# Kernel optimization log

Hardware: AMD Instinct MI355X
Metric: run time of the kernel (lower is better)

## Reference

```python
import jax, jax.numpy as jnp
import numpy as np

B, LV, LT, D, H = 32, 196, 40, 512, 8
DH = D // H


def setup_inputs() -> dict:
    key = jax.random.key(0)
    ks = jax.random.split(key, 10)
    s = 0.02
    return {
        "bef_feat": jax.random.normal(ks[0], (B, LV, D), jnp.float32),
        "sent_feat": jax.random.normal(ks[1], (B, LT, D), jnp.float32),
        "aft_feat": jax.random.normal(ks[2], (B, LV, D), jnp.float32),
        "masks": jnp.ones((B, LT), jnp.float32),
        "conv1_w": jax.random.normal(ks[3], (D, 2 * D), jnp.float32) * s,  # 1x1 conv: (out,in)
        "conv1_b": jnp.zeros((D,), jnp.float32),
        "in_proj_w": jax.random.normal(ks[4], (3 * D, D), jnp.float32) * s,
        "out_proj_w": jax.random.normal(ks[5], (D, D), jnp.float32) * s,
        "conv2_w": jax.random.normal(ks[6], (D, D), jnp.float32) * s,
        "conv2_b": jnp.zeros((D,), jnp.float32),
        "q_w": jax.random.normal(ks[7], (D, D), jnp.float32) * s,
        "q_b": jnp.zeros((D,), jnp.float32),
        "k_w": jax.random.normal(ks[8], (D, D), jnp.float32) * s,
        "k_b": jnp.zeros((D,), jnp.float32),
        "logit_scale": jnp.ones((), jnp.float32),
    }


def _forward(bef_feat, sent_feat, aft_feat, masks,
             conv1_w, conv1_b, in_proj_w, out_proj_w, conv2_w, conv2_b,
             q_w, q_b, k_w, k_b, logit_scale):
    batch, Lv, d = bef_feat.shape
    # masked text mean (plain mean over full length, as in original)
    sent = sent_feat * masks[:, :, None]
    sent_mean = jnp.mean(sent, axis=1)  # (B, D)
    # concat image grid feat with broadcast text feat -> 1x1 conv (conv1)
    img = jnp.transpose(bef_feat, (0, 2, 1))                       # (B, D, 196)
    txt = jnp.broadcast_to(sent_mean[:, :, None], (batch, d, Lv))  # (B, D, 196)
    v1 = jnp.concatenate([img, txt], axis=1)                       # (B, 2D, 196)
    v1 = jnp.einsum('bcl,oc->blo', v1, conv1_w) + conv1_b          # (B, 196, D)
    # multi-head self-attention over the 196 positions (no biases)
    qkv = jnp.einsum('bld,ed->ble', v1, in_proj_w)                 # (B, 196, 3D)
    q, k, v = jnp.split(qkv, 3, axis=-1)
    to_heads = lambda t: t.reshape(batch, Lv, H, DH).transpose(0, 2, 1, 3)
    q, k, v = to_heads(q), to_heads(k), to_heads(v)
    scores = jnp.einsum('bhld,bhmd->bhlm', q, k) / jnp.sqrt(jnp.float32(DH))
    attn = jax.nn.softmax(scores, axis=-1)
    o = jnp.einsum('bhlm,bhmd->bhld', attn, v)
    o = o.transpose(0, 2, 1, 3).reshape(batch, Lv, d)
    o = o @ out_proj_w.T
    # 1x1 conv (conv2)
    mod_img1 = jnp.einsum('bld,od->blo', o, conv2_w) + conv2_b     # (B, 196, D)
    # ContraAttention: cross-batch retrieval logits
    ql = (mod_img1 @ q_w.T + q_b).reshape(batch, Lv, H, DH).transpose(0, 2, 1, 3)  # (B,H,196,DH)
    kl = (aft_feat @ k_w.T + k_b).reshape(batch, Lv, H, DH).transpose(0, 2, 1, 3)  # (B,H,196,DH)
    logits = jnp.einsum('ahld,bhmd->ablm', ql, kl)                 # (B, B, 196, 196), sums over h,d
    # vid_mask and com_mask (attention_mask) are all-ones -> sums are Lv
    t2v = jnp.sum(jnp.max(logits, axis=-1), axis=2) / jnp.float32(Lv)  # (B, B)
    v2t = jnp.sum(jnp.max(logits, axis=-2), axis=2) / jnp.float32(Lv)  # (B, B)
    S = 0.5 * (t2v + v2t) * jnp.exp(logit_scale)
    cross_en = lambda m: -jnp.mean(jnp.diag(jax.nn.log_softmax(m, axis=-1)))
    return 0.5 * (cross_en(S) + cross_en(S.T))


def reference(bef_feat, sent_feat, aft_feat, masks,
              conv1_w, conv1_b, in_proj_w, out_proj_w, conv2_w, conv2_b,
              q_w, q_b, k_w, k_b, logit_scale):
    return _forward(bef_feat, sent_feat, aft_feat, masks,
                    conv1_w, conv1_b, in_proj_w, out_proj_w, conv2_w, conv2_b,
                    q_w, q_b, k_w, k_b, logit_scale)
```

## Files before the change

kernel.cpp:

```cpp
#include <hip/hip_runtime.h>


typedef unsigned int u32;
typedef unsigned short u16;
typedef __attribute__((ext_vector_type(8))) short bf16x8;
typedef __attribute__((ext_vector_type(4))) float f32x4;

#define DEV __device__ __forceinline__

DEV u16 f2bf(float f) {
  u32 u = __builtin_bit_cast(u32, f);
  u = (u + 0x7FFFu + ((u >> 16) & 1u)) >> 16;
  return (u16)u;
}
DEV float bf2f(u16 h) { u32 u = ((u32)h) << 16; return __builtin_bit_cast(float, u); }
DEV u32 encf(float f) { u32 u = __builtin_bit_cast(u32, f); return (u & 0x80000000u) ? ~u : (u | 0x80000000u); }
DEV float decf(u32 e) { u32 u = (e & 0x80000000u) ? (e & 0x7FFFFFFFu) : ~e; return __builtin_bit_cast(float, u); }

DEV void gll16(const u16* g, u16* l) {
  __builtin_amdgcn_global_load_lds(
      (const __attribute__((address_space(1))) void*)g,
      (__attribute__((address_space(3))) void*)l, 16, 0, 0);
}

#define VMCNT0 asm volatile("s_waitcnt vmcnt(0)" ::: "memory")
#define SBAR __builtin_amdgcn_s_barrier()

DEV void cast8(const float* __restrict__ in, u16* __restrict__ out, int i) {
  const float4* p = (const float4*)in + (size_t)i * 2;
  float4 a = p[0], b = p[1];
  u16 t[8] = {f2bf(a.x), f2bf(a.y), f2bf(a.z), f2bf(a.w),
              f2bf(b.x), f2bf(b.y), f2bf(b.z), f2bf(b.w)};
  *(uint4*)(out + (size_t)i * 8) = *(uint4*)t;
}

DEV void tcast(const float* __restrict__ in, u16* __restrict__ out, int t, int tid, float* sm) {
  int bx = t & 15, by = t >> 4;
  int tx = tid & 31, ty = tid >> 5;
  float (*tt)[33] = (float(*)[33])sm;
  for (int i = ty; i < 32; i += 8) tt[i][tx] = in[(size_t)(by * 32 + i) * 512 + bx * 32 + tx];
  __syncthreads();
  for (int i = ty; i < 32; i += 8) out[(size_t)(bx * 32 + i) * 512 + by * 32 + tx] = f2bf(tt[tx][i]);
}

__global__ __launch_bounds__(256) void k_prep(
    const float* __restrict__ bef, const float* __restrict__ aft,
    const float* __restrict__ sent, const float* __restrict__ masks,
    const float* __restrict__ conv1_w, const float* __restrict__ conv1_b,
    const float* __restrict__ in_proj_w, const float* __restrict__ out_proj_w,
    const float* __restrict__ conv2_w, const float* __restrict__ conv2_b,
    const float* __restrict__ q_w, const float* __restrict__ q_b,
    const float* __restrict__ k_w,
    u16* __restrict__ bef16, u16* __restrict__ aft16,
    u16* __restrict__ inproj16, u16* __restrict__ kw16, u16* __restrict__ qw16,
    u16* __restrict__ w1a16, u16* __restrict__ wcT16, u16* __restrict__ woT16,
    float* __restrict__ biasb, float* __restrict__ biasq,
    uint4* __restrict__ maxbuf) {
  __shared__ float smemf[1056];
  const int blk = blockIdx.x, tid = threadIdx.x;
  if (blk < 32) {
    int b = blk;
    float* sm = smemf;
    for (int d = tid; d < 512; d += 256) {
      float s = 0.f;
#pragma unroll 8
      for (int t = 0; t < 40; ++t) s += sent[(size_t)b * 40 * 512 + (size_t)t * 512 + d] * masks[b * 40 + t];
      sm[d] = s * (1.0f / 40.0f);
    }
    __syncthreads();
    for (int o = tid; o < 512; o += 256) {
      const float* wr = conv1_w + (size_t)o * 1024 + 512;
      float acc = conv1_b[o];
#pragma unroll 8
      for (int c = 0; c < 512; ++c) acc += sm[c] * wr[c];
      biasb[b * 512 + o] = acc;
    }
  } else if (blk < 424) {
    maxbuf[(size_t)(blk - 32) * 256 + tid] = (uint4){0u, 0u, 0u, 0u};
  } else if (blk < 426) {
    int j = (blk - 424) * 256 + tid;
    if (j < 512) {
      const float* wr = q_w + (size_t)j * 512;
      float acc = q_b[j];
#pragma unroll 8
      for (int d = 0; d < 512; ++d) acc += wr[d] * conv2_b[d];
      biasq[j] = acc;
    }
  } else if (blk < 1994) {
    cast8(bef, bef16, (blk - 426) * 256 + tid);
  } else if (blk < 3562) {
    cast8(aft, aft16, (blk - 1994) * 256 + tid);
  } else if (blk < 3946) {
    cast8(in_proj_w, inproj16, (blk - 3562) * 256 + tid);
  } else if (blk < 4074) {
    cast8(k_w, kw16, (blk - 3946) * 256 + tid);
  } else if (blk < 4202) {
    cast8(q_w, qw16, (blk - 4074) * 256 + tid);
  } else if (blk < 4330) {
    int i = (blk - 4202) * 256 + tid;
    int o = i >> 6, c0 = (i & 63) * 8;
    const float* p = conv1_w + (size_t)o * 1024 + c0;
    u16 t[8];
#pragma unroll
    for (int j = 0; j < 8; ++j) t[j] = f2bf(p[j]);
    *(uint4*)(w1a16 + (size_t)o * 512 + c0) = *(uint4*)t;
  } else if (blk < 4586) {
    tcast(conv2_w, wcT16, blk - 4330, tid, smemf);
  } else {
    tcast(out_proj_w, woT16, blk - 4586, tid, smemf);
  }
}

DEV void stage_gm(const u16* __restrict__ xb, const u16* __restrict__ wb,
                  u16* Xb, u16* Wb, int wave, int lane, int koff, int scol) {
  int r8 = lane >> 3;
#pragma unroll
  for (int i = 0; i < 6; ++i) {
    int s = wave + i * 4;
    if (s < 16) gll16(xb + (size_t)(s * 8 + r8) * 512 + koff + scol, Xb + s * 512);
    else        gll16(wb + (size_t)((s - 16) * 8 + r8) * 512 + koff + scol, Wb + (s - 16) * 512);
  }
}

DEV void comp_gm(const u16* Xb, const u16* Wb, int wave, int quad, int l15, int rsw,
                 f32x4 (&acc)[2][4]) {
#pragma unroll
  for (int kk = 0; kk < 64; kk += 32) {
    int co = (kk | (quad << 3)) ^ rsw;
    bf16x8 a0 = *(const bf16x8*)&Xb[(wave * 32 + l15) * 64 + co];
    bf16x8 a1 = *(const bf16x8*)&Xb[(wave * 32 + 16 + l15) * 64 + co];
#pragma unroll
    for (int nt = 0; nt < 4; ++nt) {
      bf16x8 b = *(const bf16x8*)&Wb[(nt * 16 + l15) * 64 + co];
      acc[0][nt] = __builtin_amdgcn_mfma_f32_16x16x32_bf16(a0, b, acc[0][nt], 0, 0, 0);
      acc[1][nt] = __builtin_amdgcn_mfma_f32_16x16x32_bf16(a1, b, acc[1][nt], 0, 0, 0);
    }
  }
}

__global__ __launch_bounds__(256) void k_gemm2(
    const u16* __restrict__ X1, const u16* __restrict__ W1, u16* __restrict__ o1,
    const float* __restrict__ b1, int nbx1, int N1, int m1, int nblk1,
    const u16* __restrict__ X2, const u16* __restrict__ W2, u16* __restrict__ o2,
    const float* __restrict__ b2, int nbx2, int N2, int m2) {
  __shared__ u16 Xl0[128 * 64], Xl1[128 * 64];
  __shared__ u16 Wl0[64 * 64],  Wl1[64 * 64];
  int g = blockIdx.x;
  const u16 *X, *W; u16* out; const float* bias; int N, biasMode, bx, by;
  if (g < nblk1) {
    X = X1; W = W1; out = o1; bias = b1; N = N1; biasMode = m1;
    bx = g % nbx1; by = g / nbx1;
  } else {
    g -= nblk1;
    X = X2; W = W2; out = o2; bias = b2; N = N2; biasMode = m2;
    bx = g % nbx2; by = g / nbx2;
  }
  int tid = threadIdx.x;
  int tileM = bx * 128, tileN = by * 64;
  int wave = tid >> 6, lane = tid & 63, quad = lane >> 4, l15 = lane & 15;
  const int rsw = (l15 & 7) << 3;
  const int scol = (((lane & 7) ^ ((lane >> 3) & 7)) << 3);
  f32x4 z = {0.f, 0.f, 0.f, 0.f};
  f32x4 acc[2][4] = {{z, z, z, z}, {z, z, z, z}};
  const u16* xb = X + (size_t)tileM * 512;
  const u16* wb = W + (size_t)tileN * 512;

  stage_gm(xb, wb, Xl0, Wl0, wave, lane, 0, scol);
  VMCNT0; SBAR;
#pragma unroll
  for (int kc = 0; kc < 8; kc += 2) {
    stage_gm(xb, wb, Xl1, Wl1, wave, lane, (kc + 1) * 64, scol);
    comp_gm(Xl0, Wl0, wave, quad, l15, rsw, acc);
    VMCNT0; SBAR;
    if (kc + 2 < 8)
      stage_gm(xb, wb, Xl0, Wl0, wave, lane, (kc + 2) * 64, scol);
    comp_gm(Xl1, Wl1, wave, quad, l15, rsw, acc);
    VMCNT0; SBAR;
  }
#pragma unroll
  for (int s = 0; s < 2; ++s) {
    int row0 = tileM + wave * 32 + s * 16 + quad * 4;
#pragma unroll
    for (int nt = 0; nt < 4; ++nt) {
      int col = tileN + nt * 16 + l15;
      float bv = (biasMode == 1) ? bias[col] : 0.0f;
#pragma unroll
      for (int r = 0; r < 4; ++r) {
        int row = row0 + r;
        float v = acc[s][nt][r] + bv;
        if (biasMode == 2) v += bias[(row / 196) * 512 + col];
        out[(size_t)row * N + col] = f2bf(v);
      }
    }
  }
}

__global__ __launch_bounds__(256, 1) void k_attn2(const u16* __restrict__ qkv, u16* __restrict__ o_out) {
  const int b = blockIdx.x >> 3, h = blockIdx.x & 7;
  __shared__ u16 Ks[208 * 72];
  __shared__ u16 Vt[64 * 232];
  __shared__ u16 Ps[4][16 * 232];
  const int tid = threadIdx.x;
  const int wave = tid >> 6, lane = tid & 63, quad = lane >> 4, l15 = lane & 15;
  const size_t base = (size_t)b * 196 * 1536 + (size_t)h * 64;

  for (int i = tid; i < 64 * 232 / 4; i += 256) ((unsigned long long*)Vt)[i] = 0ULL;
  for (int i = tid; i < 4 * 16 * 24; i += 256) {
    int w = i / 384, rem = i - w * 384;
    int r = rem / 24, c = rem - r * 24;
    Ps[w][r * 232 + 208 + c] = 0;
  }
  __syncthreads();

  for (int idx = tid; idx < 208 * 8; idx += 256) {
    int r = idx >> 3, c = (idx & 7) * 8;
    uint4 v = {0, 0, 0, 0};
    if (r < 196) v = *(const uint4*)&qkv[base + 512 + (size_t)r * 1536 + c];
    *(uint4*)&Ks[r * 72 + c] = v;
  }
  for (int idx = tid; idx < 196 * 8; idx += 256) {
    int p = idx >> 3, f0 = (idx & 7) * 8;
    uint4 v = *(const uint4*)&qkv[base + 1024 + (size_t)p * 1536 + f0];
    u16 t[8]; *(uint4*)t = v;
#pragma unroll
    for (int j = 0; j < 8; ++j) Vt[(f0 + j) * 232 + p] = t[j];
  }
  bf16x8 qz = {0, 0, 0, 0, 0, 0, 0, 0};
  bf16x8 qf[4][2];
#pragma unroll
  for (int i = 0; i < 4; ++i) {
    int s = wave + i * 4;
    int row = s * 16 + l15;
#pragma unroll
    for (int c = 0; c < 2; ++c) {
      bf16x8 v = qz;
      if (s < 13 && row < 196)
        v = *(const bf16x8*)&qkv[base + (size_t)row * 1536 + c * 32 + quad * 8];
      qf[i][c] = v;
    }
  }
  __syncthreads();

  const f32x4 z = {0.f, 0.f, 0.f, 0.f};
  for (int i = 0; i < 4; ++i) {
    int s = wave + i * 4;
    if (s >= 13) break;
    f32x4 acc[13];
#pragma unroll
    for (int nt = 0; nt < 13; ++nt) acc[nt] = z;
#pragma unroll
    for (int c = 0; c < 2; ++c) {
      bf16x8 a = qf[i][c];
#pragma unroll
      for (int nt = 0; nt < 13; ++nt) {
        bf16x8 bfr = *(const bf16x8*)&Ks[(nt * 16 + l15) * 72 + c * 32 + quad * 8];
        acc[nt] = __builtin_amdgcn_mfma_f32_16x16x32_bf16(a, bfr, acc[nt], 0, 0, 0);
      }
    }
#pragma unroll
    for (int r = 0; r < 4; ++r) {
      float m = -3e38f;
#pragma unroll
      for (int nt = 0; nt < 13; ++nt) {
        float sv = acc[nt][r] * 0.125f;
        acc[nt][r] = sv;
        if (nt < 12 || l15 < 4) m = fmaxf(m, sv);
      }
#pragma unroll
      for (int off = 1; off < 16; off <<= 1) m = fmaxf(m, __shfl_xor(m, off));
      float ssum = 0.f;
#pragma unroll
      for (int nt = 0; nt < 13; ++nt) {
        float p = (nt < 12 || l15 < 4) ? __expf(acc[nt][r] - m) : 0.f;
        acc[nt][r] = p;
        ssum += p;
      }
#pragma unroll
      for (int off = 1; off < 16; off <<= 1) ssum += __shfl_xor(ssum, off);
      float is = 1.0f / ssum;
      int row = quad * 4 + r;
#pragma unroll
      for (int nt = 0; nt < 13; ++nt) {
        float v = acc[nt][r] * is;
        float vx = __shfl_xor(v, 1);
        if ((l15 & 1) == 0) {
          u32 pk = (u32)f2bf(v) | ((u32)f2bf(vx) << 16);
          *(u32*)&Ps[wave][row * 232 + nt * 16 + l15] = pk;
        }
      }
    }
    f32x4 oacc[4] = {z, z, z, z};
#pragma unroll
    for (int kc = 0; kc < 7; ++kc) {
      bf16x8 a = *(const bf16x8*)&Ps[wave][l15 * 232 + kc * 32 + quad * 8];
#pragma unroll
      for (int nt = 0; nt < 4; ++nt) {
        bf16x8 bfr = *(const bf16x8*)&Vt[(nt * 16 + l15) * 232 + kc * 32 + quad * 8];
        oacc[nt] = __builtin_amdgcn_mfma_f32_16x16x32_bf16(a, bfr, oacc[nt], 0, 0, 0);
      }
    }
#pragma unroll
    for (int nt = 0; nt < 4; ++nt) {
#pragma unroll
      for (int r = 0; r < 4; ++r) {
        int row = s * 16 + quad * 4 + r;
        if (row < 196)
          o_out[((size_t)b * 196 + row) * 512 + h * 64 + nt * 16 + l15] = f2bf(oacc[nt][r]);
      }
    }
  }
}

DEV void stage_lg(const u16* __restrict__ qbase, const u16* __restrict__ kbase,
                  u16* Qb, u16* Kb, int wave, int lane, int koff, int scol) {
  int r4 = lane >> 2;
#pragma unroll
  for (int i = 0; i < 6; ++i) {
    int s = wave + i * 4;
    if (s < 8) {
      gll16(qbase + (size_t)(s * 16 + r4) * 512 + koff + scol, Qb + s * 512);
    } else if (s < 21) {
      int j = s - 8;
      int r = j * 16 + r4; if (r > 195) r = 195;
      gll16(kbase + (size_t)r * 512 + koff + scol, Kb + j * 512);
    }
  }
}

DEV void comp_lg(const u16* Qb, const u16* Kb, int wave, int l15, int co, f32x4 (&acc)[2][13]) {
  bf16x8 af0 = *(const bf16x8*)&Qb[(wave * 16 + l15) * 32 + co];
  bf16x8 af1 = *(const bf16x8*)&Qb[((wave + 4) * 16 + l15) * 32 + co];
  __builtin_amdgcn_s_setprio(1);
#pragma unroll
  for (int nt = 0; nt < 13; ++nt) {
    bf16x8 b = *(const bf16x8*)&Kb[(nt * 16 + l15) * 32 + co];
    acc[0][nt] = __builtin_amdgcn_mfma_f32_16x16x32_bf16(af0, b, acc[0][nt], 0, 0, 0);
    acc[1][nt] = __builtin_amdgcn_mfma_f32_16x16x32_bf16(af1, b, acc[1][nt], 0, 0, 0);
  }
  __builtin_amdgcn_s_setprio(0);
}

#define WAIT_W() do { \
    if (wave == 0) asm volatile("s_waitcnt vmcnt(6)" ::: "memory"); \
    else           asm volatile("s_waitcnt vmcnt(5)" ::: "memory"); \
  } while (0)

__global__ __launch_bounds__(256) void k_logits2(const u16* __restrict__ QL, const u16* __restrict__ KL,
                                                 u32* __restrict__ rowmax, u32* __restrict__ colmax) {
  int lin = blockIdx.y * 49 + blockIdx.x;
  lin = (lin & 7) * 196 + (lin >> 3);
  const int bx = lin % 49, b = lin / 49;
  const int row0 = bx * 128;
  __shared__ u16 Qb0[128 * 32], Qb1[128 * 32], Qb2[128 * 32];
  __shared__ u16 Kb0[208 * 32], Kb1[208 * 32], Kb2[208 * 32];
  __shared__ float colred[2][4 * 208];
  const int tid = threadIdx.x;
  const int wave = tid >> 6, lane = tid & 63, quad = lane >> 4, l15 = lane & 15;
  const int scol = (((lane & 3) ^ ((lane >> 3) & 3)) << 3);
  const int co = ((quad ^ ((l15 >> 1) & 3)) << 3);
  const int a0 = row0 / 196;
  const int lsplit = (a0 + 1) * 196 - row0;
  const f32x4 z = {0.f, 0.f, 0.f, 0.f};
  f32x4 acc[2][13];
#pragma unroll
  for (int s = 0; s < 2; ++s)
#pragma unroll
    for (int nt = 0; nt < 13; ++nt) acc[s][nt] = z;
  const u16* qbase = QL + (size_t)row0 * 512;
  const u16* kbase = KL + (size_t)b * 196 * 512;

  u16 *qa = Qb0, *qb = Qb1, *qc = Qb2;
  u16 *ka = Kb0, *kb = Kb1, *kc = Kb2;
  stage_lg(qbase, kbase, qa, ka, wave, lane, 0, scol);
  stage_lg(qbase, kbase, qb, kb, wave, lane, 32, scol);
  for (int t = 0; t < 14; ++t) {
    WAIT_W();
    SBAR;
    stage_lg(qbase, kbase, qc, kc, wave, lane, (t + 2) * 32, scol);
    comp_lg(qa, ka, wave, l15, co, acc);
    u16* tq = qa; qa = qb; qb = qc; qc = tq;
    u16* tk = ka; ka = kb; kb = kc; kc = tk;
  }
  WAIT_W(); SBAR;
  comp_lg(qa, ka, wave, l15, co, acc);
  { u16* tq = qa; qa = qb; qb = qc; qc = tq;
    u16* tk = ka; ka = kb; kb = kc; kc = tk; }
  VMCNT0; SBAR;
  comp_lg(qa, ka, wave, l15, co, acc);

#pragma unroll
  for (int s = 0; s < 2; ++s) {
#pragma unroll
    for (int r = 0; r < 4; ++r) {
      float m = -3e38f;
#pragma unroll
      for (int nt = 0; nt < 13; ++nt)
        if (nt < 12 || l15 < 4) m = fmaxf(m, acc[s][nt][r]);
#pragma unroll
      for (int off = 8; off > 0; off >>= 1) m = fmaxf(m, __shfl_xor(m, off, 16));
      if (l15 == 0) {
        int lr = (wave + s * 4) * 16 + quad * 4 + r;
        int aa = a0, ll = row0 - a0 * 196 + lr;
        if (ll >= 196) { aa += 1; ll -= 196; }
        atomicMax(&rowmax[((size_t)aa * 32 + b) * 196 + ll], encf(m));
      }
    }
  }
#pragma unroll
  for (int nt = 0; nt < 13; ++nt) {
    float cm0 = -3e38f, cm1 = -3e38f;
#pragma unroll
    for (int s = 0; s < 2; ++s)
#pragma unroll
      for (int r = 0; r < 4; ++r) {
        int lr = (wave + s * 4) * 16 + quad * 4 + r;
        float v = acc[s][nt][r];
        if (lr < lsplit) cm0 = fmaxf(cm0, v); else cm1 = fmaxf(cm1, v);
      }
    cm0 = fmaxf(cm0, __shfl_xor(cm0, 16)); cm0 = fmaxf(cm0, __shfl_xor(cm0, 32));
    cm1 = fmaxf(cm1, __shfl_xor(cm1, 16)); cm1 = fmaxf(cm1, __shfl_xor(cm1, 32));
    if (quad == 0) {
      colred[0][wave * 208 + nt * 16 + l15] = cm0;
      colred[1][wave * 208 + nt * 16 + l15] = cm1;
    }
  }
  __syncthreads();
  for (int c = tid; c < 196; c += 256) {
    float m0 = fmaxf(fmaxf(colred[0][c], colred[0][208 + c]), fmaxf(colred[0][416 + c], colred[0][624 + c]));
    atomicMax(&colmax[((size_t)a0 * 32 + b) * 196 + c], encf(m0));
    if (lsplit < 128) {
      float m1 = fmaxf(fmaxf(colred[1][c], colred[1][208 + c]), fmaxf(colred[1][416 + c], colred[1][624 + c]));
      atomicMax(&colmax[((size_t)(a0 + 1) * 32 + b) * 196 + c], encf(m1));
    }
  }
}

__global__ __launch_bounds__(1024) void k_final(const u32* __restrict__ maxbuf,
                                                const float* __restrict__ logit_scale, float* __restrict__ out) {
  __shared__ float S[1024];
  __shared__ float terms[64];
  int tid = threadIdx.x;
  float sc = 0.5f * __expf(logit_scale[0]);
  const uint4* rp = (const uint4*)(maxbuf + (size_t)tid * 196);
  const uint4* cp = (const uint4*)(maxbuf + 200704 + (size_t)tid * 196);
  float s = 0.f;
#pragma unroll 7
  for (int i = 0; i < 49; ++i) {
    uint4 v = rp[i]; s += decf(v.x) + decf(v.y) + decf(v.z) + decf(v.w);
    uint4 w = cp[i]; s += decf(w.x) + decf(w.y) + decf(w.z) + decf(w.w);
  }
  S[tid] = sc * s * (1.0f / 196.0f);
  __syncthreads();
  if (tid < 64) {
    int aa = tid & 31;
    bool rowMode = tid < 32;
    float mx = -3e38f;
    for (int j = 0; j < 32; ++j) {
      float v = rowMode ? S[aa * 32 + j] : S[j * 32 + aa];
      mx = fmaxf(mx, v);
    }
    float se = 0.f;
    for (int j = 0; j < 32; ++j) {
      float v = rowMode ? S[aa * 32 + j] : S[j * 32 + aa];
      se += __expf(v - mx);
    }
    terms[tid] = S[aa * 33] - (mx + logf(se));
  }
  __syncthreads();
  if (tid == 0) {
    float s2 = 0.f;
    for (int i = 0; i < 64; ++i) s2 += terms[i];
    out[0] = -s2 * (1.0f / 64.0f);
  }
}

extern "C" void kernel_launch(void* const* d_in, const int* in_sizes, int n_in,
                              void* d_out, int out_size, void* d_ws, size_t ws_size,
                              hipStream_t stream) {
  const float* bef       = (const float*)d_in[0];
  const float* sent      = (const float*)d_in[1];
  const float* aft       = (const float*)d_in[2];
  const float* masks     = (const float*)d_in[3];
  const float* conv1_w   = (const float*)d_in[4];
  const float* conv1_b   = (const float*)d_in[5];
  const float* in_proj_w = (const float*)d_in[6];
  const float* out_proj_w= (const float*)d_in[7];
  const float* conv2_w   = (const float*)d_in[8];
  const float* conv2_b   = (const float*)d_in[9];
  const float* q_w       = (const float*)d_in[10];
  const float* q_b       = (const float*)d_in[11];
  const float* k_w       = (const float*)d_in[12];
  const float* k_b       = (const float*)d_in[13];
  const float* logit_scale = (const float*)d_in[14];
  float* out = (float*)d_out;

  char* ws = (char*)d_ws;
  size_t off = 0;
  auto alloc = [&](size_t bytes) -> char* {
    char* p = ws + off;
    off += (bytes + 255) & ~(size_t)255;
    return p;
  };
  const size_t MROWS = 32 * 196;
  u16* bef16    = (u16*)alloc(MROWS * 512 * 2);
  u16* aft16    = (u16*)alloc(MROWS * 512 * 2);
  u16* w1a16    = (u16*)alloc(512 * 512 * 2);
  u16* inproj16 = (u16*)alloc(1536 * 512 * 2);
  u16* kw16     = (u16*)alloc(512 * 512 * 2);
  u16* qw16     = (u16*)alloc(512 * 512 * 2);
  u16* wcT16    = (u16*)alloc(512 * 512 * 2);
  u16* woT16    = (u16*)alloc(512 * 512 * 2);
  u16* wt16     = (u16*)alloc(512 * 512 * 2);
  u16* wcomb16  = (u16*)alloc(512 * 512 * 2);
  float* biasb  = (float*)alloc(32 * 512 * 4);
  float* biasq  = (float*)alloc(512 * 4);
  u16* v116     = (u16*)alloc(MROWS * 512 * 2);
  u16* qkv16    = (u16*)alloc(MROWS * 1536 * 2);
  u16* oattn16  = (u16*)alloc(MROWS * 512 * 2);
  u16* QL16     = (u16*)alloc(MROWS * 512 * 2);
  u16* KL16     = (u16*)alloc(MROWS * 512 * 2);
  u32* maxbuf   = (u32*)alloc(2 * 32 * 32 * 196 * 4);
  u32* rowmax   = maxbuf;
  u32* colmax   = maxbuf + 32 * 32 * 196;

  k_prep<<<4842, 256, 0, stream>>>(bef, aft, sent, masks, conv1_w, conv1_b,
                                   in_proj_w, out_proj_w, conv2_w, conv2_b,
                                   q_w, q_b, k_w,
                                   bef16, aft16, inproj16, kw16, qw16,
                                   w1a16, wcT16, woT16, biasb, biasq,
                                   (uint4*)maxbuf);
  k_gemm2<<<424, 256, 0, stream>>>(bef16, w1a16, v116, biasb, 49, 512, 2, 392,
                                   qw16, wcT16, wt16, nullptr, 4, 512, 0);
  k_gemm2<<<1208, 256, 0, stream>>>(v116, inproj16, qkv16, nullptr, 49, 1536, 0, 1176,
                                    wt16, woT16, wcomb16, nullptr, 4, 512, 0);
  k_attn2<<<256, 256, 0, stream>>>(qkv16, oattn16);
  k_gemm2<<<784, 256, 0, stream>>>(oattn16, wcomb16, QL16, biasq, 49, 512, 1, 392,
                                   aft16, kw16, KL16, k_b, 49, 512, 1);
  k_logits2<<<dim3(49, 32), 256, 0, stream>>>(QL16, KL16, rowmax, colmax);
  k_final<<<1, 1024, 0, stream>>>(maxbuf, logit_scale, out);
}
```

Baseline: 401.8 us.

## Enlarge GEMM tiles to 128x128, split attention by query half, parallelize final reduction

The GEMM kernel now uses 128x128 output tiles with a 2x2 wave layout and 4x4 MFMA accumulators, which halves block counts and doubles reuse of the staged operands. Attention blocks are split into two halves over query row tiles, giving 512 blocks to raise occupancy, though each block still stages the full K and V. The final reduction over max buffers moves from a single 1024-thread block to a separate multi-block wave-reduction kernel. In exchange, accumulator register pressure rises, K/V loading is duplicated, and there is one more kernel launch.

```diff
diff --git a/kernel.cpp b/kernel.cpp
--- a/kernel.cpp
+++ b/kernel.cpp
@@ -111,40 +111,43 @@
   }
 }
 
-DEV void stage_gm(const u16* __restrict__ xb, const u16* __restrict__ wb,
+DEV void stage_g3(const u16* __restrict__ xb, const u16* __restrict__ wb,
                   u16* Xb, u16* Wb, int wave, int lane, int koff, int scol) {
   int r8 = lane >> 3;
 #pragma unroll
-  for (int i = 0; i < 6; ++i) {
+  for (int i = 0; i < 8; ++i) {
     int s = wave + i * 4;
     if (s < 16) gll16(xb + (size_t)(s * 8 + r8) * 512 + koff + scol, Xb + s * 512);
     else        gll16(wb + (size_t)((s - 16) * 8 + r8) * 512 + koff + scol, Wb + (s - 16) * 512);
   }
 }
 
-DEV void comp_gm(const u16* Xb, const u16* Wb, int wave, int quad, int l15, int rsw,
-                 f32x4 (&acc)[2][4]) {
+DEV void comp_g3(const u16* Xb, const u16* Wb, int wr, int wc, int quad, int l15, int rsw,
+                 f32x4 (&acc)[4][4]) {
 #pragma unroll
   for (int kk = 0; kk < 64; kk += 32) {
     int co = (kk | (quad << 3)) ^ rsw;
-    bf16x8 a0 = *(const bf16x8*)&Xb[(wave * 32 + l15) * 64 + co];
-    bf16x8 a1 = *(const bf16x8*)&Xb[(wave * 32 + 16 + l15) * 64 + co];
+    bf16x8 af[4];
+#pragma unroll
+    for (int s = 0; s < 4; ++s)
+      af[s] = *(const bf16x8*)&Xb[(wr * 64 + s * 16 + l15) * 64 + co];
 #pragma unroll
     for (int nt = 0; nt < 4; ++nt) {
-      bf16x8 b = *(const bf16x8*)&Wb[(nt * 16 + l15) * 64 + co];
-      acc[0][nt] = __builtin_amdgcn_mfma_f32_16x16x32_bf16(a0, b, acc[0][nt], 0, 0, 0);
-      acc[1][nt] = __builtin_amdgcn_mfma_f32_16x16x32_bf16(a1, b, acc[1][nt], 0, 0, 0);
-    }
-  }
-}
-
-__global__ __launch_bounds__(256) void k_gemm2(
+      bf16x8 b = *(const bf16x8*)&Wb[(wc * 64 + nt * 16 + l15) * 64 + co];
+#pragma unroll
+      for (int s = 0; s < 4; ++s)
+        acc[s][nt] = __builtin_amdgcn_mfma_f32_16x16x32_bf16(af[s], b, acc[s][nt], 0, 0, 0);
+    }
+  }
+}
+
+__global__ __launch_bounds__(256) void k_gemm3d(
     const u16* __restrict__ X1, const u16* __restrict__ W1, u16* __restrict__ o1,
     const float* __restrict__ b1, int nbx1, int N1, int m1, int nblk1,
     const u16* __restrict__ X2, const u16* __restrict__ W2, u16* __restrict__ o2,
     const float* __restrict__ b2, int nbx2, int N2, int m2) {
   __shared__ u16 Xl0[128 * 64], Xl1[128 * 64];
-  __shared__ u16 Wl0[64 * 64],  Wl1[64 * 64];
+  __shared__ u16 Wl0[128 * 64], Wl1[128 * 64];
   int g = blockIdx.x;
   const u16 *X, *W; u16* out; const float* bias; int N, biasMode, bx, by;
   if (g < nblk1) {
@@ -156,33 +159,38 @@
     bx = g % nbx2; by = g / nbx2;
   }
   int tid = threadIdx.x;
-  int tileM = bx * 128, tileN = by * 64;
+  int tileM = bx * 128, tileN = by * 128;
   int wave = tid >> 6, lane = tid & 63, quad = lane >> 4, l15 = lane & 15;
+  int wr = wave >> 1, wc = wave & 1;
   const int rsw = (l15 & 7) << 3;
   const int scol = (((lane & 7) ^ ((lane >> 3) & 7)) << 3);
   f32x4 z = {0.f, 0.f, 0.f, 0.f};
-  f32x4 acc[2][4] = {{z, z, z, z}, {z, z, z, z}};
+  f32x4 acc[4][4];
+#pragma unroll
+  for (int s = 0; s < 4; ++s)
+#pragma unroll
+    for (int nt = 0; nt < 4; ++nt) acc[s][nt] = z;
   const u16* xb = X + (size_t)tileM * 512;
   const u16* wb = W + (size_t)tileN * 512;
 
-  stage_gm(xb, wb, Xl0, Wl0, wave, lane, 0, scol);
+  stage_g3(xb, wb, Xl0, Wl0, wave, lane, 0, scol);
   VMCNT0; SBAR;
 #pragma unroll
   for (int kc = 0; kc < 8; kc += 2) {
-    stage_gm(xb, wb, Xl1, Wl1, wave, lane, (kc + 1) * 64, scol);
-    comp_gm(Xl0, Wl0, wave, quad, l15, rsw, acc);
+    stage_g3(xb, wb, Xl1, Wl1, wave, lane, (kc + 1) * 64, scol);
+    comp_g3(Xl0, Wl0, wr, wc, quad, l15, rsw, acc);
     VMCNT0; SBAR;
     if (kc + 2 < 8)
-      stage_gm(xb, wb, Xl0, Wl0, wave, lane, (kc + 2) * 64, scol);
-    comp_gm(Xl1, Wl1, wave, quad, l15, rsw, acc);
+      stage_g3(xb, wb, Xl0, Wl0, wave, lane, (kc + 2) * 64, scol);
+    comp_g3(Xl1, Wl1, wr, wc, quad, l15, rsw, acc);
     VMCNT0; SBAR;
   }
 #pragma unroll
-  for (int s = 0; s < 2; ++s) {
-    int row0 = tileM + wave * 32 + s * 16 + quad * 4;
+  for (int s = 0; s < 4; ++s) {
+    int row0 = tileM + wr * 64 + s * 16 + quad * 4;
 #pragma unroll
     for (int nt = 0; nt < 4; ++nt) {
-      int col = tileN + nt * 16 + l15;
+      int col = tileN + wc * 64 + nt * 16 + l15;
       float bv = (biasMode == 1) ? bias[col] : 0.0f;
 #pragma unroll
       for (int r = 0; r < 4; ++r) {
@@ -196,7 +204,9 @@
 }
 
 __global__ __launch_bounds__(256, 1) void k_attn2(const u16* __restrict__ qkv, u16* __restrict__ o_out) {
-  const int b = blockIdx.x >> 3, h = blockIdx.x & 7;
+  const int blk = blockIdx.x;
+  const int b = blk >> 4, h = (blk >> 1) & 7, half = blk & 1;
+  const int sb = half * 8, se = half ? 13 : 8;
   __shared__ u16 Ks[208 * 72];
   __shared__ u16 Vt[64 * 232];
   __shared__ u16 Ps[4][16 * 232];
@@ -226,15 +236,15 @@
     for (int j = 0; j < 8; ++j) Vt[(f0 + j) * 232 + p] = t[j];
   }
   bf16x8 qz = {0, 0, 0, 0, 0, 0, 0, 0};
-  bf16x8 qf[4][2];
-#pragma unroll
-  for (int i = 0; i < 4; ++i) {
-    int s = wave + i * 4;
+  bf16x8 qf[2][2];
+#pragma unroll
+  for (int i = 0; i < 2; ++i) {
+    int s = sb + wave + i * 4;
     int row = s * 16 + l15;
 #pragma unroll
     for (int c = 0; c < 2; ++c) {
       bf16x8 v = qz;
-      if (s < 13 && row < 196)
+      if (s < se && row < 196)
         v = *(const bf16x8*)&qkv[base + (size_t)row * 1536 + c * 32 + quad * 8];
       qf[i][c] = v;
     }
@@ -242,9 +252,9 @@
   __syncthreads();
 
   const f32x4 z = {0.f, 0.f, 0.f, 0.f};
-  for (int i = 0; i < 4; ++i) {
-    int s = wave + i * 4;
-    if (s >= 13) break;
+  for (int i = 0; i < 2; ++i) {
+    int s = sb + wave + i * 4;
+    if (s >= se) break;
     f32x4 acc[13];
 #pragma unroll
     for (int nt = 0; nt < 13; ++nt) acc[nt] = z;
@@ -435,21 +445,25 @@
   }
 }
 
-__global__ __launch_bounds__(1024) void k_final(const u32* __restrict__ maxbuf,
+__global__ __launch_bounds__(256) void k_sred(const u32* __restrict__ maxbuf, float* __restrict__ Sws) {
+  int wave = threadIdx.x >> 6, lane = threadIdx.x & 63;
+  int p = blockIdx.x * 4 + wave;
+  const u32* rp = maxbuf + (size_t)p * 196;
+  const u32* cp = maxbuf + 200704 + (size_t)p * 196;
+  float s = 0.f;
+  for (int i = lane; i < 196; i += 64) s += decf(rp[i]) + decf(cp[i]);
+#pragma unroll
+  for (int off = 1; off < 64; off <<= 1) s += __shfl_xor(s, off);
+  if (lane == 0) Sws[p] = s;
+}
+
+__global__ __launch_bounds__(1024) void k_final(const float* __restrict__ Sws,
                                                 const float* __restrict__ logit_scale, float* __restrict__ out) {
   __shared__ float S[1024];
   __shared__ float terms[64];
   int tid = threadIdx.x;
   float sc = 0.5f * __expf(logit_scale[0]);
-  const uint4* rp = (const uint4*)(maxbuf + (size_t)tid * 196);
-  const uint4* cp = (const uint4*)(maxbuf + 200704 + (size_t)tid * 196);
-  float s = 0.f;
-#pragma unroll 7
-  for (int i = 0; i < 49; ++i) {
-    uint4 v = rp[i]; s += decf(v.x) + decf(v.y) + decf(v.z) + decf(v.w);
-    uint4 w = cp[i]; s += decf(w.x) + decf(w.y) + decf(w.z) + decf(w.w);
-  }
-  S[tid] = sc * s * (1.0f / 196.0f);
+  S[tid] = sc * Sws[tid] * (1.0f / 196.0f);
   __syncthreads();
   if (tid < 64) {
     int aa = tid & 31;
@@ -520,6 +534,7 @@
   u16* QL16     = (u16*)alloc(MROWS * 512 * 2);
   u16* KL16     = (u16*)alloc(MROWS * 512 * 2);
   u32* maxbuf   = (u32*)alloc(2 * 32 * 32 * 196 * 4);
+  float* Sws    = (float*)alloc(1024 * 4);
   u32* rowmax   = maxbuf;
   u32* colmax   = maxbuf + 32 * 32 * 196;
 
@@ -529,13 +544,14 @@
                                    bef16, aft16, inproj16, kw16, qw16,
                                    w1a16, wcT16, woT16, biasb, biasq,
                                    (uint4*)maxbuf);
-  k_gemm2<<<424, 256, 0, stream>>>(bef16, w1a16, v116, biasb, 49, 512, 2, 392,
-                                   qw16, wcT16, wt16, nullptr, 4, 512, 0);
-  k_gemm2<<<1208, 256, 0, stream>>>(v116, inproj16, qkv16, nullptr, 49, 1536, 0, 1176,
+  k_gemm3d<<<212, 256, 0, stream>>>(bef16, w1a16, v116, biasb, 49, 512, 2, 196,
+                                    qw16, wcT16, wt16, nullptr, 4, 512, 0);
+  k_gemm3d<<<604, 256, 0, stream>>>(v116, inproj16, qkv16, nullptr, 49, 1536, 0, 588,
                                     wt16, woT16, wcomb16, nullptr, 4, 512, 0);
-  k_attn2<<<256, 256, 0, stream>>>(qkv16, oattn16);
-  k_gemm2<<<784, 256, 0, stream>>>(oattn16, wcomb16, QL16, biasq, 49, 512, 1, 392,
-                                   aft16, kw16, KL16, k_b, 49, 512, 1);
+  k_attn2<<<512, 256, 0, stream>>>(qkv16, oattn16);
+  k_gemm3d<<<392, 256, 0, stream>>>(oattn16, wcomb16, QL16, biasq, 49, 512, 1, 196,
+                                    aft16, kw16, KL16, k_b, 49, 512, 1);
   k_logits2<<<dim3(49, 32), 256, 0, stream>>>(QL16, KL16, rowmax, colmax);
-  k_final<<<1, 1024, 0, stream>>>(maxbuf, logit_scale, out);
-}
+  k_sred<<<256, 256, 0, stream>>>(maxbuf, Sws);
+  k_final<<<1, 1024, 0, stream>>>(Sws, logit_scale, out);
+}
```

After: 331.8 us (median of 2 runs). 1.21x faster.
